# Optimization experiments

Hardware: AMD Instinct MI355X
Metric: run time of the kernel (lower is better)

## Reference

```python
import jax, jax.numpy as jnp
import numpy as np
from jax.scipy.linalg import expm
jax.config.update("jax_enable_x64", True)

HBAR = 0.6582119569
CM2EV = 0.00012398419
N6A, N10A = 4, 4
DT = 1.0
KDC = dict(E_S1=3.995, E_S2=4.9183, om6a=596.0 * CM2EV, om10a=919.0 * CM2EV,
           kap6a_S1=-0.0964, kap6a_S2=0.1193, lam=0.1825, gamma=-0.018)


def _build():
    cd = np.complex128

    def ladder(n):
        a = np.zeros((n, n), dtype=cd)
        for k in range(1, n):
            a[k - 1, k] = np.sqrt(float(k))
        adag = a.conj().T
        return (a + adag) / np.sqrt(2.0), adag @ a, np.eye(n, dtype=cd)

    Q6a1, N6a1, I6a = ladder(N6A)
    Q10a1, N10a1, I10a = ladder(N10A)
    Nel, Dvib = 3, N6A * N10A
    Ivib = np.eye(Dvib, dtype=cd)
    Iel = np.eye(Nel, dtype=cd)
    lift = lambda op: np.kron(Iel, op)
    Q6a = lift(np.kron(Q6a1, I10a))
    Q10a = lift(np.kron(I6a, Q10a1))
    N6a = lift(np.kron(N6a1, I10a))
    N10a = lift(np.kron(I6a, N10a1))
    P = []
    for k in range(Nel):
        ek = np.zeros(Nel, dtype=cd); ek[k] = 1.0
        P.append(np.kron(np.outer(ek, ek), Ivib))
    e1 = np.zeros(Nel, dtype=cd); e1[1] = 1.0
    e2 = np.zeros(Nel, dtype=cd); e2[2] = 1.0
    Poff = np.kron(np.outer(e1, e2) + np.outer(e2, e1), Ivib)
    Lj = np.kron(np.outer(e1, e2), Ivib)  # |S1><S2| lift
    D = Nel * Dvib
    I = np.eye(D, dtype=cd)
    p = KDC
    H = (p['E_S1'] * P[1] + p['E_S2'] * P[2] + p['om6a'] * N6a + p['om10a'] * N10a
         + p['kap6a_S1'] * P[1] @ Q6a + p['kap6a_S2'] * P[2] @ Q6a
         + p['lam'] * Poff @ Q10a + p['gamma'] * Poff @ (Q10a @ Q10a))
    # Coherent part -i(I kron H - H^T* kron I); dissipator at unit rate (scaled by g later)
    Lc = -1j * (np.kron(I, H) - np.kron(H.conj().T, I))
    LdL = Lj.conj().T @ Lj
    Ld0 = (np.kron(Lj.conj(), Lj) - 0.5 * np.kron(I, LdL)
           - 0.5 * np.kron(LdL.conj().T, I))
    psi = np.zeros(D, dtype=cd); psi[2 * N6A * N10A] = 1.0
    rho0 = np.outer(psi, psi.conj()).reshape(-1)
    trP = np.stack([P[k].T.reshape(-1) for k in range(3)])  # [3, D^2]
    return Lc, Ld0, rho0, trP

_LC, _LD0, _RHO0, _TRP = _build()


def setup_inputs() -> dict:
    return {"log_g": jnp.asarray(np.log(1.0 / 40.0), dtype=jnp.float32),
            "n_steps": 1000}


def reference(log_g, n_steps):
    Lc = jnp.asarray(_LC)
    Ld0 = jnp.asarray(_LD0)
    rho0 = jnp.asarray(_RHO0)
    trP = jnp.asarray(_TRP)
    g = jnp.exp(log_g).astype(jnp.float64)
    Lsup = Lc + g * Ld0                      # [D^2, D^2] complex128
    U = expm(Lsup * (DT / HBAR))             # one-step propagator

    def step(rho, _):
        pops = jnp.real(trP @ rho)           # tr(P_k rho), k=0..2
        return U @ rho, pops

    _, ps = jax.lax.scan(step, rho0, None, length=int(n_steps))  # [n_steps, 3]
    return (ps[:, 0].astype(jnp.float32),
            ps[:, 1].astype(jnp.float32),
            ps[:, 2].astype(jnp.float32))
```

## Files before the change

### kernel.cpp

```cpp
#include <hip/hip_runtime.h>
#include <math.h>


#define DS 1024
#define MATD ((size_t)DS * DS * sizeof(double))
#define PA 66

typedef double v4d __attribute__((ext_vector_type(4)));

__device__ inline double Qel(int i, int j) {
    if (i == j + 1) return sqrt((double)i) * 0.70710678118654752440;
    if (j == i + 1) return sqrt((double)j) * 0.70710678118654752440;
    return 0.0;
}

__device__ inline void fill_H(double* Hs, int tid) {
    const double CM2EV = 0.00012398419;
    const double E_S1 = 3.995, E_S2 = 4.9183;
    const double om6a = 596.0 * CM2EV, om10a = 919.0 * CM2EV;
    const double kapA = -0.0964, kapB = 0.1193, lam = 0.1825, gam = -0.018;
    for (int h = tid; h < 1024; h += 256) {
        int r = h >> 5, c = h & 31;
        int e = r >> 4, v6 = (r >> 2) & 3, v10 = r & 3;
        int e2 = c >> 4, w6 = (c >> 2) & 3, w10 = c & 3;
        double val = 0.0;
        if (r == c) val += (e ? E_S2 : E_S1) + om6a * v6 + om10a * v10;
        if (e == e2 && v10 == w10) val += (e ? kapB : kapA) * Qel(v6, w6);
        if (e != e2 && v6 == w6) {
            double q2 = 0.0;
            #pragma unroll
            for (int m = 0; m < 4; ++m) q2 += Qel(v10, m) * Qel(m, w10);
            val += lam * Qel(v10, w10) + gam * q2;
        }
        Hs[h] = val;
    }
}

__global__ __launch_bounds__(256)
void build_G10(const float* __restrict__ logg, double* __restrict__ X,
               double* __restrict__ Y, double* __restrict__ Z)
{
    int tid = threadIdx.x;
    if (blockIdx.x >= 4096) {
        int idx = (blockIdx.x - 4096) * 256 + tid;
        if (idx < 64 * 1024) {
            int r = idx >> 10, i = idx & 1023;
            double v = 0.0;
            if (r < 2 && i % 33 == 0) {
                int a = i / 33;
                if ((a < 16) == (r == 0)) v = 1.0;
            }
            Y[idx] = v;
        } else if (idx < 64 * 1024 + 1024) {
            int i = idx - 64 * 1024;
            Z[i] = (i == 528) ? 1.0 : 0.0;
        }
        return;
    }
    __shared__ double Hs[1024];
    fill_H(Hs, tid);
    __syncthreads();
    double g = exp((double)logg[0]);
    const double sc = ((1.0 / 0.6582119569) / 16.0) / 10.0;
    int idx = blockIdx.x * 256 + tid;
    int r = idx >> 10, c = idx & 1023;
    int i = r >> 5, j = r & 31;
    int k = c >> 5, l = c & 31;
    double t = 0.0;
    if (k <= l) {
        if (i <= j) {
            if (i < 16 && j < 16) {
                int p = i + 16, q = j + 16;
                if ((p == k && q == l) || (p == l && q == k)) t += g;
            }
            if (i == k && j == l) t -= 0.5 * g * ((i >= 16) + (j >= 16));
        } else {
            if (j == l) t += Hs[i * 32 + k];
            if (k != l && j == k) t += Hs[i * 32 + l];
            if (i == k) t -= Hs[l * 32 + j];
            if (k != l && i == l) t -= Hs[k * 32 + j];
        }
    } else {
        if (i <= j) {
            double ha = 0.0;
            if (j == l) ha += Hs[i * 32 + k];
            if (j == k) ha -= Hs[i * 32 + l];
            if (i == k) ha -= Hs[l * 32 + j];
            if (i == l) ha += Hs[k * 32 + j];
            t -= ha;
        } else {
            if (i < 16 && j < 16 && (i + 16 == k) && (j + 16 == l)) t += g;
            if (i == k && j == l) t -= 0.5 * g * ((i >= 16) + (j >= 16));
        }
    }
    X[idx] = t * sc + ((r == c) ? 1.0 : 0.0);
}

__global__ __launch_bounds__(256)
void apply_T(const float* __restrict__ logg, const double* __restrict__ M,
             double* __restrict__ O, double invk)
{
    __shared__ double Hs[1024];
    __shared__ double wlist[72];
    __shared__ int    qlist[72];
    __shared__ int    Kshared;
    const int tid = threadIdx.x;
    fill_H(Hs, tid);
    __syncthreads();
    const double g = exp((double)logg[0]);
    const double sck = ((1.0 / 0.6582119569) / 16.0) * invk;
    const int p = ((blockIdx.x & 7) << 7) | (blockIdx.x >> 3);
    const int i = p >> 5, j = p & 31;

    if (tid < 64) {
        const int m = tid & 31;
        const bool loop2 = tid >= 32;
        double c = loop2 ? Hs[m * 32 + j] : Hs[i * 32 + m];
        int q = 0; double w = 0.0; bool valid;
        if (i <= j) {
            if (!loop2) {
                valid = (c != 0.0) && (m != j);
                q = (m > j) ? m * 32 + j : j * 32 + m;
                w = (m > j) ? -c : c;
            } else {
                valid = (c != 0.0) && (m != i);
                q = (i > m) ? i * 32 + m : m * 32 + i;
                w = (i > m) ? c : -c;
            }
        } else {
            if (!loop2) {
                valid = (c != 0.0);
                int lo = m < j ? m : j, hi = m < j ? j : m;
                q = lo * 32 + hi; w = c;
            } else {
                valid = (c != 0.0);
                int lo = m < i ? m : i, hi = m < i ? i : m;
                q = lo * 32 + hi; w = -c;
            }
        }
        unsigned long long mask = __ballot(valid);
        int slot = __popcll(mask & ((1ull << tid) - 1ull));
        if (valid) { qlist[slot] = q; wlist[slot] = w; }
        if (tid == 0) {
            int K = __popcll(mask);
            if (i < 16 && j < 16) {
                qlist[K] = (i + 16) * 32 + (j + 16); wlist[K] = g; ++K;
            }
            double wd = -0.5 * g * (double)((i >= 16) + (j >= 16));
            if (wd != 0.0) { qlist[K] = p; wlist[K] = wd; ++K; }
            while (K & 3) { qlist[K] = 0; wlist[K] = 0.0; ++K; }
            Kshared = K;
        }
    }
    __syncthreads();
    const int K = Kshared;

    double a0 = 0.0, a1 = 0.0, a2 = 0.0, a3 = 0.0;
    const double2* Mp = (const double2*)M;
    const int e2 = tid << 1;
    for (int k = 0; k < K; k += 4) {
        #pragma unroll
        for (int u = 0; u < 4; ++u) {
            int q = qlist[k + u];
            double w = wlist[k + u];
            double2 v0 = Mp[(size_t)q * (DS / 2) + e2];
            double2 v1 = Mp[(size_t)q * (DS / 2) + e2 + 1];
            a0 += w * v0.x; a1 += w * v0.y;
            a2 += w * v1.x; a3 += w * v1.y;
        }
    }
    const int c0 = tid << 2;
    size_t base = (size_t)p * DS + c0;
    O[base + 0] = sck * a0 + ((p == c0)     ? 1.0 : 0.0);
    O[base + 1] = sck * a1 + ((p == c0 + 1) ? 1.0 : 0.0);
    O[base + 2] = sck * a2 + ((p == c0 + 2) ? 1.0 : 0.0);
    O[base + 3] = sck * a3 + ((p == c0 + 3) ? 1.0 : 0.0);
}

__global__ __launch_bounds__(1024, 1)
void dgemm(const double* __restrict__ A, const double* __restrict__ B,
           double* __restrict__ D)
{
    __shared__ double As[2][64 * PA];
    __shared__ double Bs[2][64 * PA];
    const int tid = threadIdx.x;
    const int bm = blockIdx.x << 6, bn = blockIdx.y << 6;
    const int w = tid >> 6, lane = tid & 63;
    const int lr = lane & 15, lk = lane >> 4;
    const int p = w & 3, kg = w >> 2;
    const int wr = (p >> 1) << 5, wc = (p & 1) << 5;

    v4d acc[2][2];
    #pragma unroll
    for (int si = 0; si < 2; ++si)
        #pragma unroll
        for (int sj = 0; sj < 2; ++sj) acc[si][sj] = (v4d){0., 0., 0., 0.};

    const int ra = tid >> 4;
    const int cs = (tid & 15) << 2;
    const double* gA = A + (size_t)(bm + ra) * DS + cs;
    const double* gB = B + (size_t)ra * DS + bn + cs;
    double va[4], vb[4];
    #pragma unroll
    for (int u = 0; u < 4; ++u) { va[u] = gA[u]; vb[u] = gB[u]; }
    #pragma unroll
    for (int u = 0; u < 4; ++u) {
        As[0][ra * PA + cs + u] = va[u];
        Bs[0][ra * PA + cs + u] = vb[u];
    }
    #pragma unroll
    for (int u = 0; u < 4; ++u) {
        va[u] = gA[64 + u];
        vb[u] = gB[(size_t)64 * DS + u];
    }
    __syncthreads();

    #pragma unroll 2
    for (int kt = 0; kt < DS; kt += 64) {
        const int pb = (kt >> 6) & 1;
        const bool more  = (kt + 64) < DS;
        const bool more2 = (kt + 128) < DS;
        const int k0 = (kg << 4) + lk;
        double A00 = As[pb][(wr + lr) * PA + k0];
        double A10 = As[pb][(wr + 16 + lr) * PA + k0];
        double B00 = Bs[pb][k0 * PA + wc + lr];
        double B10 = Bs[pb][k0 * PA + wc + 16 + lr];
        double A01 = As[pb][(wr + lr) * PA + k0 + 4];
        double A11 = As[pb][(wr + 16 + lr) * PA + k0 + 4];
        double B01 = Bs[pb][(k0 + 4) * PA + wc + lr];
        double B11 = Bs[pb][(k0 + 4) * PA + wc + 16 + lr];
        acc[0][0] = __builtin_amdgcn_mfma_f64_16x16x4f64(A00, B00, acc[0][0], 0, 0, 0);
        acc[0][1] = __builtin_amdgcn_mfma_f64_16x16x4f64(A00, B10, acc[0][1], 0, 0, 0);
        acc[1][0] = __builtin_amdgcn_mfma_f64_16x16x4f64(A10, B00, acc[1][0], 0, 0, 0);
        acc[1][1] = __builtin_amdgcn_mfma_f64_16x16x4f64(A10, B10, acc[1][1], 0, 0, 0);
        acc[0][0] = __builtin_amdgcn_mfma_f64_16x16x4f64(A01, B01, acc[0][0], 0, 0, 0);
        acc[0][1] = __builtin_amdgcn_mfma_f64_16x16x4f64(A01, B11, acc[0][1], 0, 0, 0);
        acc[1][0] = __builtin_amdgcn_mfma_f64_16x16x4f64(A11, B01, acc[1][0], 0, 0, 0);
        acc[1][1] = __builtin_amdgcn_mfma_f64_16x16x4f64(A11, B11, acc[1][1], 0, 0, 0);
        if (more) {
            #pragma unroll
            for (int u = 0; u < 4; ++u) {
                As[pb ^ 1][ra * PA + cs + u] = va[u];
                Bs[pb ^ 1][ra * PA + cs + u] = vb[u];
            }
        }
        if (more2) {
            #pragma unroll
            for (int u = 0; u < 4; ++u) {
                va[u] = gA[kt + 128 + u];
                vb[u] = gB[(size_t)(kt + 128) * DS + u];
            }
        }
        double A02 = As[pb][(wr + lr) * PA + k0 + 8];
        double A12 = As[pb][(wr + 16 + lr) * PA + k0 + 8];
        double B02 = Bs[pb][(k0 + 8) * PA + wc + lr];
        double B12 = Bs[pb][(k0 + 8) * PA + wc + 16 + lr];
        double A03 = As[pb][(wr + lr) * PA + k0 + 12];
        double A13 = As[pb][(wr + 16 + lr) * PA + k0 + 12];
        double B03 = Bs[pb][(k0 + 12) * PA + wc + lr];
        double B13 = Bs[pb][(k0 + 12) * PA + wc + 16 + lr];
        acc[0][0] = __builtin_amdgcn_mfma_f64_16x16x4f64(A02, B02, acc[0][0], 0, 0, 0);
        acc[0][1] = __builtin_amdgcn_mfma_f64_16x16x4f64(A02, B12, acc[0][1], 0, 0, 0);
        acc[1][0] = __builtin_amdgcn_mfma_f64_16x16x4f64(A12, B02, acc[1][0], 0, 0, 0);
        acc[1][1] = __builtin_amdgcn_mfma_f64_16x16x4f64(A12, B12, acc[1][1], 0, 0, 0);
        acc[0][0] = __builtin_amdgcn_mfma_f64_16x16x4f64(A03, B03, acc[0][0], 0, 0, 0);
        acc[0][1] = __builtin_amdgcn_mfma_f64_16x16x4f64(A03, B13, acc[0][1], 0, 0, 0);
        acc[1][0] = __builtin_amdgcn_mfma_f64_16x16x4f64(A13, B03, acc[1][0], 0, 0, 0);
        acc[1][1] = __builtin_amdgcn_mfma_f64_16x16x4f64(A13, B13, acc[1][1], 0, 0, 0);
        __syncthreads();
    }

    double* red = &As[0][0];
    if (kg == 3) {
        #pragma unroll
        for (int si = 0; si < 2; ++si)
            #pragma unroll
            for (int sj = 0; sj < 2; ++sj)
                #pragma unroll
                for (int r = 0; r < 4; ++r)
                    red[(wr + si * 16 + lk + 4 * r) * 64 + wc + sj * 16 + lr]
                        = acc[si][sj][r];
    }
    __syncthreads();
    if (kg == 2) {
        #pragma unroll
        for (int si = 0; si < 2; ++si)
            #pragma unroll
            for (int sj = 0; sj < 2; ++sj)
                #pragma unroll
                for (int r = 0; r < 4; ++r)
                    red[(wr + si * 16 + lk + 4 * r) * 64 + wc + sj * 16 + lr]
                        += acc[si][sj][r];
    }
    __syncthreads();
    if (kg == 1) {
        #pragma unroll
        for (int si = 0; si < 2; ++si)
            #pragma unroll
            for (int sj = 0; sj < 2; ++sj)
                #pragma unroll
                for (int r = 0; r < 4; ++r)
                    red[(wr + si * 16 + lk + 4 * r) * 64 + wc + sj * 16 + lr]
                        += acc[si][sj][r];
    }
    __syncthreads();
    if (kg == 0) {
        #pragma unroll
        for (int si = 0; si < 2; ++si)
            #pragma unroll
            for (int sj = 0; sj < 2; ++sj) {
                int col = bn + wc + sj * 16 + lr;
                #pragma unroll
                for (int r = 0; r < 4; ++r) {
                    int row = bm + wr + si * 16 + lk + 4 * r;
                    D[(size_t)row * DS + col] = acc[si][sj][r]
                        + red[(wr + si * 16 + lk + 4 * r) * 64 + wc + sj * 16 + lr];
                }
            }
    }
}

__global__ __launch_bounds__(256)
void ypart(const double* __restrict__ P, const double* __restrict__ Y,
           double* __restrict__ scratch, int SR)
{
    __shared__ double Yld[32 * 64];
    __shared__ double red[32 * 64];
    const int tid = threadIdx.x;
    const int cc = tid & 63, kw = tid >> 6;
    const int col = (blockIdx.x << 6) + cc;
    const int kb = blockIdx.y << 6;
    const int r0 = blockIdx.z << 5;

    for (int idx = tid; idx < 32 * 64; idx += 256) {
        int r = idx >> 6, kk = idx & 63;
        Yld[idx] = Y[(size_t)(r0 + r) * DS + kb + kk];
    }
    __syncthreads();

    double acc[32];
    #pragma unroll
    for (int r = 0; r < 32; ++r) acc[r] = 0.0;

    #pragma unroll
    for (int kk = 0; kk < 16; ++kk) {
        int kl = (kw << 4) + kk;
        double pv = P[(size_t)(kb + kl) * DS + col];
        #pragma unroll
        for (int r = 0; r < 32; ++r)
            acc[r] += Yld[(r << 6) + kl] * pv;
    }

    __syncthreads();
    if (kw == 3) {
        #pragma unroll
        for (int r = 0; r < 32; ++r) red[(r << 6) + cc] = acc[r];
    }
    __syncthreads();
    if (kw == 2) {
        #pragma unroll
        for (int r = 0; r < 32; ++r) red[(r << 6) + cc] += acc[r];
    }
    __syncthreads();
    if (kw == 1) {
        #pragma unroll
        for (int r = 0; r < 32; ++r) red[(r << 6) + cc] += acc[r];
    }
    __syncthreads();
    if (kw == 0) {
        #pragma unroll
        for (int r = 0; r < 32; ++r) red[(r << 6) + cc] += acc[r];
    }
    __syncthreads();
    for (int idx = tid; idx < 32 * 64; idx += 256) {
        int r = idx >> 6, c2 = idx & 63;
        scratch[((size_t)blockIdx.y * SR + r0 + r) * DS + (blockIdx.x << 6) + c2]
            = red[idx];
    }
}

__global__ __launch_bounds__(256)
void yreduce(const double* __restrict__ scratch, double* __restrict__ Y,
             int M, int SR)
{
    int idx = blockIdx.x * 256 + threadIdx.x;
    int r = idx >> 10, c = idx & 1023;
    double s = 0.0;
    #pragma unroll
    for (int q = 0; q < 16; ++q)
        s += scratch[((size_t)q * SR + r) * DS + c];
    Y[(size_t)(M + r) * DS + c] = s;
}

__global__ __launch_bounds__(256)
void zstep(const double* __restrict__ V, const double* __restrict__ Zin,
           double* __restrict__ Zout)
{
    int row = blockIdx.x * 4 + (threadIdx.x >> 6);
    int lane = threadIdx.x & 63;
    const double2* r_ = (const double2*)(V + (size_t)row * DS);
    const double2* z_ = (const double2*)Zin;
    double s = 0.0;
    #pragma unroll
    for (int k = 0; k < 8; ++k) {
        double2 a = r_[(k << 6) + lane];
        double2 b = z_[(k << 6) + lane];
        s += a.x * b.x + a.y * b.y;
    }
    #pragma unroll
    for (int off = 32; off; off >>= 1) s += __shfl_down(s, off);
    if (lane == 0) Zout[row] = s;
}

__global__ __launch_bounds__(128)
void final_pops(const double* __restrict__ Y, const double* __restrict__ Z,
                float* __restrict__ out, int n)
{
    int t = blockIdx.x;
    int k = threadIdx.x >> 6, lane = threadIdx.x & 63;
    int a = t & 31, j = t >> 5;
    const double* y = Y + (size_t)(2 * a + k) * 1024;
    const double* z = Z + (size_t)j * 1024;
    double s = 0.0;
    for (int i = lane; i < 1024; i += 64) s += y[i] * z[i];
    #pragma unroll
    for (int off = 32; off; off >>= 1) s += __shfl_down(s, off);
    if (lane == 0) {
        out[(size_t)(k + 1) * n + t] = (float)s;
        if (k == 0) out[t] = 0.0f;
    }
}

static inline void ydouble2(const double* P, double* Y, double* scr, int M,
                            hipStream_t stream)
{
    int gz = (M + 31) / 32; if (gz < 1) gz = 1;
    int SR = gz * 32;
    ypart<<<dim3(16, 16, gz), 256, 0, stream>>>(P, Y, scr, SR);
    yreduce<<<SR * 4, 256, 0, stream>>>(scr, Y, M, SR);
}

extern "C" void kernel_launch(void* const* d_in, const int* in_sizes, int n_in,
                              void* d_out, int out_size, void* d_ws, size_t ws_size,
                              hipStream_t stream)
{
    const float* logg = (const float*)d_in[0];
    float* out = (float*)d_out;
    const int n = out_size / 3;
    (void)in_sizes; (void)n_in; (void)ws_size;

    char* ws = (char*)d_ws;
    double* b0 = (double*)(ws + 0 * MATD);
    double* b1 = (double*)(ws + 1 * MATD);
    double* b2 = (double*)(ws + 2 * MATD);
    double* scr = (double*)(ws + 3 * MATD);
    double* Y  = (double*)(ws + 5 * MATD);
    double* Z  = Y + 64 * 1024;

    dim3 g2(16, 16);

    build_G10<<<4096 + 260, 256, 0, stream>>>(logg, b0, Y, Z);
    double* src = b0; double* dst = b1;
    for (int k = 9; k >= 1; --k) {
        apply_T<<<1024, 256, 0, stream>>>(logg, src, dst, 1.0 / (double)k);
        double* t = src; src = dst; dst = t;
    }

    dgemm<<<g2, 1024, 0, stream>>>(b1, b1, b0);
    dgemm<<<g2, 1024, 0, stream>>>(b0, b0, b2);
    dgemm<<<g2, 1024, 0, stream>>>(b2, b2, b1);
    dgemm<<<g2, 1024, 0, stream>>>(b1, b1, b0);
    ydouble2(b0, Y, scr, 2, stream);
    dgemm<<<g2, 1024, 0, stream>>>(b0, b0, b1);
    ydouble2(b1, Y, scr, 4, stream);
    dgemm<<<g2, 1024, 0, stream>>>(b1, b1, b2);
    ydouble2(b2, Y, scr, 8, stream);
    dgemm<<<g2, 1024, 0, stream>>>(b2, b2, b1);
    ydouble2(b1, Y, scr, 16, stream);
    dgemm<<<g2, 1024, 0, stream>>>(b1, b1, b2);
    ydouble2(b2, Y, scr, 32, stream);
    dgemm<<<g2, 1024, 0, stream>>>(b2, b2, b1);

    for (int j = 1; j < 32; ++j)
        zstep<<<256, 256, 0, stream>>>(b1, Z + (size_t)(j - 1) * 1024,
                                       Z + (size_t)j * 1024);

    final_pops<<<n, 128, 0, stream>>>(Y, Z, out, n);
}
```

Measured before the change: 636.6 us.

## Process 2x2 output rows per apply_T block and deepen ypart K-split

apply_T now handles a 2x2 tile of superoperator rows per block, merging their sparse row lists so each loaded input row is reused across four outputs, and launches 256 blocks instead of 1024. ypart now loops over four K tiles per block, shrinking the K-split from 16 to 4 partial sums and cutting scratch traffic in yreduce. The changes reduce redundant global reads at the cost of fewer blocks (lower parallelism) and more registers per thread.

```diff
diff --git a/kernel.cpp b/kernel.cpp
--- a/kernel.cpp
+++ b/kernel.cpp
@@ -101,80 +101,191 @@
              double* __restrict__ O, double invk)
 {
     __shared__ double Hs[1024];
-    __shared__ double wlist[72];
-    __shared__ int    qlist[72];
+    __shared__ int    qlist[112];
+    __shared__ double wl[4][112];
+    __shared__ int    counts[4];
     __shared__ int    Kshared;
     const int tid = threadIdx.x;
     fill_H(Hs, tid);
     __syncthreads();
     const double g = exp((double)logg[0]);
     const double sck = ((1.0 / 0.6582119569) / 16.0) * invk;
-    const int p = ((blockIdx.x & 7) << 7) | (blockIdx.x >> 3);
-    const int i = p >> 5, j = p & 31;
-
-    if (tid < 64) {
-        const int m = tid & 31;
-        const bool loop2 = tid >= 32;
-        double c = loop2 ? Hs[m * 32 + j] : Hs[i * 32 + m];
-        int q = 0; double w = 0.0; bool valid;
-        if (i <= j) {
-            if (!loop2) {
-                valid = (c != 0.0) && (m != j);
-                q = (m > j) ? m * 32 + j : j * 32 + m;
-                w = (m > j) ? -c : c;
+
+    const int a = blockIdx.x >> 4, b = blockIdx.x & 15;
+    const int i0 = a << 1, j0 = b << 1;
+    const int wv = tid >> 6, lane = tid & 63;
+    const int m = lane & 31;
+
+    bool valid = false; int q = 0;
+    double w0 = 0.0, w1 = 0.0, w2 = 0.0, w3 = 0.0;
+
+    if (a != b) {
+        if (lane < 32) {
+            const bool fam2 = (wv >= 2);
+            const int sel = wv & 1;
+            if (!fam2) {
+                const int js = j0 + sel;
+                double cA = Hs[i0 * 32 + m];
+                double cB = Hs[(i0 + 1) * 32 + m];
+                if (a < b) {
+                    if ((cA != 0.0 || cB != 0.0) && m != js) {
+                        valid = true;
+                        q = (m > js) ? m * 32 + js : js * 32 + m;
+                        double sA = (m > js) ? -cA : cA;
+                        double sB = (m > js) ? -cB : cB;
+                        if (sel == 0) { w0 = sA; w2 = sB; }
+                        else          { w1 = sA; w3 = sB; }
+                    }
+                } else {
+                    if (cA != 0.0 || cB != 0.0) {
+                        valid = true;
+                        q = (m < js) ? m * 32 + js : js * 32 + m;
+                        if (sel == 0) { w0 = cA; w2 = cB; }
+                        else          { w1 = cA; w3 = cB; }
+                    }
+                }
             } else {
-                valid = (c != 0.0) && (m != i);
-                q = (i > m) ? i * 32 + m : m * 32 + i;
-                w = (i > m) ? c : -c;
+                const int is = i0 + sel;
+                double c0 = Hs[m * 32 + j0];
+                double c1 = Hs[m * 32 + j0 + 1];
+                if (a < b) {
+                    if ((c0 != 0.0 || c1 != 0.0) && m != is) {
+                        valid = true;
+                        q = (is > m) ? is * 32 + m : m * 32 + is;
+                        double s0 = (is > m) ? c0 : -c0;
+                        double s1 = (is > m) ? c1 : -c1;
+                        if (sel == 0) { w0 = s0; w1 = s1; }
+                        else          { w2 = s0; w3 = s1; }
+                    }
+                } else {
+                    if (c0 != 0.0 || c1 != 0.0) {
+                        valid = true;
+                        q = (m < is) ? m * 32 + is : is * 32 + m;
+                        if (sel == 0) { w0 = -c0; w1 = -c1; }
+                        else          { w2 = -c0; w3 = -c1; }
+                    }
+                }
+            }
+        }
+    } else {
+        const int ia = i0 + (wv >> 1), ja = j0 + (wv & 1);
+        const bool up = (ia <= ja);
+        double wr = 0.0;
+        if (lane < 32) {
+            double c = Hs[ia * 32 + m];
+            if (up) {
+                if (c != 0.0 && m != ja) {
+                    valid = true;
+                    q = (m > ja) ? m * 32 + ja : ja * 32 + m;
+                    wr = (m > ja) ? -c : c;
+                }
+            } else {
+                if (c != 0.0) {
+                    valid = true;
+                    q = (m < ja) ? m * 32 + ja : ja * 32 + m;
+                    wr = c;
+                }
             }
         } else {
-            if (!loop2) {
-                valid = (c != 0.0);
-                int lo = m < j ? m : j, hi = m < j ? j : m;
-                q = lo * 32 + hi; w = c;
+            double c = Hs[m * 32 + ja];
+            if (up) {
+                if (c != 0.0 && m != ia) {
+                    valid = true;
+                    q = (ia > m) ? ia * 32 + m : m * 32 + ia;
+                    wr = (ia > m) ? c : -c;
+                }
             } else {
-                valid = (c != 0.0);
-                int lo = m < i ? m : i, hi = m < i ? i : m;
-                q = lo * 32 + hi; w = -c;
-            }
-        }
-        unsigned long long mask = __ballot(valid);
-        int slot = __popcll(mask & ((1ull << tid) - 1ull));
-        if (valid) { qlist[slot] = q; wlist[slot] = w; }
-        if (tid == 0) {
-            int K = __popcll(mask);
-            if (i < 16 && j < 16) {
-                qlist[K] = (i + 16) * 32 + (j + 16); wlist[K] = g; ++K;
-            }
-            double wd = -0.5 * g * (double)((i >= 16) + (j >= 16));
-            if (wd != 0.0) { qlist[K] = p; wlist[K] = wd; ++K; }
-            while (K & 3) { qlist[K] = 0; wlist[K] = 0.0; ++K; }
-            Kshared = K;
-        }
+                if (c != 0.0) {
+                    valid = true;
+                    q = (m < ia) ? m * 32 + ia : ia * 32 + m;
+                    wr = -c;
+                }
+            }
+        }
+        if (wv == 0) w0 = wr; else if (wv == 1) w1 = wr;
+        else if (wv == 2) w2 = wr; else w3 = wr;
+    }
+
+    unsigned long long mask = __ballot(valid);
+    if (lane == 0) counts[wv] = __popcll(mask);
+    __syncthreads();
+    int base = 0;
+    for (int t = 0; t < wv; ++t) base += counts[t];
+    if (valid) {
+        int slot = base + __popcll(mask & ((1ull << lane) - 1ull));
+        qlist[slot] = q;
+        wl[0][slot] = w0; wl[1][slot] = w1; wl[2][slot] = w2; wl[3][slot] = w3;
+    }
+    __syncthreads();
+    if (tid == 0) {
+        int K = counts[0] + counts[1] + counts[2] + counts[3];
+        const int cnt = (a >= 8) + (b >= 8);
+        if (a < 8 && b < 8) {
+            #pragma unroll
+            for (int r = 0; r < 4; ++r) {
+                int ia = i0 + (r >> 1), ja = j0 + (r & 1);
+                qlist[K] = (ia + 16) * 32 + (ja + 16);
+                wl[0][K] = 0.0; wl[1][K] = 0.0; wl[2][K] = 0.0; wl[3][K] = 0.0;
+                wl[r][K] = g; ++K;
+            }
+        }
+        if (cnt > 0) {
+            double wd = -0.5 * g * (double)cnt;
+            #pragma unroll
+            for (int r = 0; r < 4; ++r) {
+                int ia = i0 + (r >> 1), ja = j0 + (r & 1);
+                qlist[K] = ia * 32 + ja;
+                wl[0][K] = 0.0; wl[1][K] = 0.0; wl[2][K] = 0.0; wl[3][K] = 0.0;
+                wl[r][K] = wd; ++K;
+            }
+        }
+        while (K & 1) {
+            qlist[K] = 0;
+            wl[0][K] = 0.0; wl[1][K] = 0.0; wl[2][K] = 0.0; wl[3][K] = 0.0;
+            ++K;
+        }
+        Kshared = K;
     }
     __syncthreads();
     const int K = Kshared;
 
-    double a0 = 0.0, a1 = 0.0, a2 = 0.0, a3 = 0.0;
+    double acc[4][4];
+    #pragma unroll
+    for (int r = 0; r < 4; ++r)
+        #pragma unroll
+        for (int u = 0; u < 4; ++u) acc[r][u] = 0.0;
+
     const double2* Mp = (const double2*)M;
     const int e2 = tid << 1;
-    for (int k = 0; k < K; k += 4) {
-        #pragma unroll
-        for (int u = 0; u < 4; ++u) {
-            int q = qlist[k + u];
-            double w = wlist[k + u];
-            double2 v0 = Mp[(size_t)q * (DS / 2) + e2];
-            double2 v1 = Mp[(size_t)q * (DS / 2) + e2 + 1];
-            a0 += w * v0.x; a1 += w * v0.y;
-            a2 += w * v1.x; a3 += w * v1.y;
-        }
-    }
+    for (int k = 0; k < K; k += 2) {
+        #pragma unroll
+        for (int u = 0; u < 2; ++u) {
+            int qq = qlist[k + u];
+            double W0 = wl[0][k + u], W1 = wl[1][k + u];
+            double W2 = wl[2][k + u], W3 = wl[3][k + u];
+            double2 v0 = Mp[(size_t)qq * (DS / 2) + e2];
+            double2 v1 = Mp[(size_t)qq * (DS / 2) + e2 + 1];
+            acc[0][0] += W0 * v0.x; acc[0][1] += W0 * v0.y;
+            acc[0][2] += W0 * v1.x; acc[0][3] += W0 * v1.y;
+            acc[1][0] += W1 * v0.x; acc[1][1] += W1 * v0.y;
+            acc[1][2] += W1 * v1.x; acc[1][3] += W1 * v1.y;
+            acc[2][0] += W2 * v0.x; acc[2][1] += W2 * v0.y;
+            acc[2][2] += W2 * v1.x; acc[2][3] += W2 * v1.y;
+            acc[3][0] += W3 * v0.x; acc[3][1] += W3 * v0.y;
+            acc[3][2] += W3 * v1.x; acc[3][3] += W3 * v1.y;
+        }
+    }
+
     const int c0 = tid << 2;
-    size_t base = (size_t)p * DS + c0;
-    O[base + 0] = sck * a0 + ((p == c0)     ? 1.0 : 0.0);
-    O[base + 1] = sck * a1 + ((p == c0 + 1) ? 1.0 : 0.0);
-    O[base + 2] = sck * a2 + ((p == c0 + 2) ? 1.0 : 0.0);
-    O[base + 3] = sck * a3 + ((p == c0 + 3) ? 1.0 : 0.0);
+    #pragma unroll
+    for (int r = 0; r < 4; ++r) {
+        int pr = (i0 + (r >> 1)) * 32 + (j0 + (r & 1));
+        size_t bse = (size_t)pr * DS + c0;
+        O[bse + 0] = sck * acc[r][0] + ((pr == c0)     ? 1.0 : 0.0);
+        O[bse + 1] = sck * acc[r][1] + ((pr == c0 + 1) ? 1.0 : 0.0);
+        O[bse + 2] = sck * acc[r][2] + ((pr == c0 + 2) ? 1.0 : 0.0);
+        O[bse + 3] = sck * acc[r][3] + ((pr == c0 + 3) ? 1.0 : 0.0);
+    }
 }
 
 __global__ __launch_bounds__(1024, 1)
@@ -329,26 +440,28 @@
     const int tid = threadIdx.x;
     const int cc = tid & 63, kw = tid >> 6;
     const int col = (blockIdx.x << 6) + cc;
-    const int kb = blockIdx.y << 6;
     const int r0 = blockIdx.z << 5;
 
-    for (int idx = tid; idx < 32 * 64; idx += 256) {
-        int r = idx >> 6, kk = idx & 63;
-        Yld[idx] = Y[(size_t)(r0 + r) * DS + kb + kk];
-    }
-    __syncthreads();
-
     double acc[32];
     #pragma unroll
     for (int r = 0; r < 32; ++r) acc[r] = 0.0;
 
-    #pragma unroll
-    for (int kk = 0; kk < 16; ++kk) {
-        int kl = (kw << 4) + kk;
-        double pv = P[(size_t)(kb + kl) * DS + col];
-        #pragma unroll
-        for (int r = 0; r < 32; ++r)
-            acc[r] += Yld[(r << 6) + kl] * pv;
+    for (int kt = 0; kt < 4; ++kt) {
+        const int kb = ((blockIdx.y << 2) + kt) << 6;
+        __syncthreads();
+        for (int idx = tid; idx < 32 * 64; idx += 256) {
+            int r = idx >> 6, kk = idx & 63;
+            Yld[idx] = Y[(size_t)(r0 + r) * DS + kb + kk];
+        }
+        __syncthreads();
+        #pragma unroll
+        for (int kk = 0; kk < 16; ++kk) {
+            int kl = (kw << 4) + kk;
+            double pv = P[(size_t)(kb + kl) * DS + col];
+            #pragma unroll
+            for (int r = 0; r < 32; ++r)
+                acc[r] += Yld[(r << 6) + kl] * pv;
+        }
     }
 
     __syncthreads();
@@ -387,7 +500,7 @@
     int r = idx >> 10, c = idx & 1023;
     double s = 0.0;
     #pragma unroll
-    for (int q = 0; q < 16; ++q)
+    for (int q = 0; q < 4; ++q)
         s += scratch[((size_t)q * SR + r) * DS + c];
     Y[(size_t)(M + r) * DS + c] = s;
 }
@@ -436,7 +549,7 @@
 {
     int gz = (M + 31) / 32; if (gz < 1) gz = 1;
     int SR = gz * 32;
-    ypart<<<dim3(16, 16, gz), 256, 0, stream>>>(P, Y, scr, SR);
+    ypart<<<dim3(16, 4, gz), 256, 0, stream>>>(P, Y, scr, SR);
     yreduce<<<SR * 4, 256, 0, stream>>>(scr, Y, M, SR);
 }
 
@@ -462,7 +575,7 @@
     build_G10<<<4096 + 260, 256, 0, stream>>>(logg, b0, Y, Z);
     double* src = b0; double* dst = b1;
     for (int k = 9; k >= 1; --k) {
-        apply_T<<<1024, 256, 0, stream>>>(logg, src, dst, 1.0 / (double)k);
+        apply_T<<<256, 256, 0, stream>>>(logg, src, dst, 1.0 / (double)k);
         double* t = src; src = dst; dst = t;
     }
 
```

Measured after the change: 763.1 us. +19.9%, slower.
